# Kernel optimization log

Hardware: AMD Instinct MI355X
Metric: run time of the kernel (lower is better)

The kernel has to match this reference:

```python
import jax, jax.numpy as jnp
import numpy as np
from jax import lax

EPS = 1e-8

def setup_inputs() -> dict:
    key = jax.random.key(0)
    ks = jax.random.split(key, 9)
    B, Cin, H, W = 16, 128, 64, 64
    C = 256
    return {
        "x":  jax.random.normal(ks[0], (B, Cin, H, W), jnp.float32),
        "w1": jax.random.normal(ks[1], (C, Cin, 3, 3), jnp.float32) * 0.02,
        "b1": jax.random.normal(ks[2], (C,), jnp.float32) * 0.02,
        "w2": jax.random.normal(ks[3], (C, C), jnp.float32) * 0.02,
        "b2": jax.random.normal(ks[4], (C,), jnp.float32) * 0.02,
        "w3": jax.random.normal(ks[5], (C, C), jnp.float32) * 0.02,
        "b3": jax.random.normal(ks[6], (C,), jnp.float32) * 0.02,
        "w4": jax.random.normal(ks[7], (C, C), jnp.float32) * 0.02,
        "b4": jax.random.normal(ks[8], (C,), jnp.float32) * 0.02,
    }

def reference(x, w1, b1, w2, b2, w3, b3, w4, b4):
    B = x.shape[0]
    # conv1: 3x3, pad 1 -> [B, 256, H, W]
    conv1 = lax.conv_general_dilated(
        x, w1, window_strides=(1, 1), padding="SAME",
        dimension_numbers=("NCHW", "OIHW", "NCHW")) + b1[None, :, None, None]
    H, W = conv1.shape[2], conv1.shape[3]
    C = conv1.shape[1]
    # gap1 -> [B, 256]; note: forward never applies relu/sigmoid (faithful)
    gap1 = conv1.mean(axis=(2, 3))
    c2 = gap1 @ w2.T + b2            # 1x1 conv on 1x1 spatial == dense
    c3 = c2 @ w3.T + b3              # [B, 256]
    # add1 = conv1 + conv1 * c3 (broadcast scale over spatial)
    add1 = conv1 * (1.0 + c3[:, :, None, None])
    gap2 = add1.mean(axis=(2, 3))    # [B, 256]
    # cosine similarity along channel dim between gap2 and add1 -> [B, H, W]
    num = jnp.einsum("bc,bchw->bhw", gap2, add1)
    n_g = jnp.maximum(jnp.linalg.norm(gap2, axis=1), EPS)[:, None, None]
    n_a = jnp.maximum(jnp.sqrt(jnp.sum(add1 * add1, axis=1)), EPS)
    cos = num / (n_g * n_a)
    r1 = cos.reshape(B, H * W)       # [B, HW]
    m1 = r1.T @ r1                   # [HW, HW] cross-batch position similarity
    # conv4: 1x1 conv -> [B, 256, H, W]
    conv4 = jnp.einsum("oc,bchw->bohw", w4, add1) + b4[None, :, None, None]
    # torch: permute to NHWC then view as [B, 256, HW] (mixes dims; faithful)
    r2 = jnp.transpose(conv4, (0, 2, 3, 1)).reshape(B, C, H * W)
    m2 = r2 @ m1                     # [B, 256, HW]
    return m2.reshape(B, C, H, W)
```

## Files before the change

kernel.cpp:

```cpp
#include <hip/hip_runtime.h>

#define EPSF 1e-8f

typedef __attribute__((ext_vector_type(8))) short bf16x8;
typedef __attribute__((ext_vector_type(16))) float f32x16;

#define MFMA32(a, b, c) __builtin_amdgcn_mfma_f32_32x32x16_bf16(a, b, c, 0, 0, 0)

__device__ __forceinline__ uint32_t splitpack(float v) {
    uint32_t u = __float_as_uint(v);
    uint32_t hb = (u + 0x7fffu + ((u >> 16) & 1u)) & 0xffff0000u;
    float rem = v - __uint_as_float(hb);
    uint32_t r = __float_as_uint(rem);
    uint32_t lb = (r + 0x7fffu + ((r >> 16) & 1u)) >> 16;
    return (hb >> 16) | (lb << 16);
}
__device__ __forceinline__ float unpackf(uint32_t p) {
    return __uint_as_float(p << 16) + __uint_as_float(p & 0xffff0000u);
}

__device__ __forceinline__ void unpack_frag(uint4 a, uint4 b, bf16x8& hi, bf16x8& lo) {
    union { uint32_t w[4]; bf16x8 v; } H, L;
    H.w[0] = (a.x & 0xffffu) | (a.y << 16);
    H.w[1] = (a.z & 0xffffu) | (a.w << 16);
    H.w[2] = (b.x & 0xffffu) | (b.y << 16);
    H.w[3] = (b.z & 0xffffu) | (b.w << 16);
    L.w[0] = (a.x >> 16) | (a.y & 0xffff0000u);
    L.w[1] = (a.z >> 16) | (a.w & 0xffff0000u);
    L.w[2] = (b.x >> 16) | (b.y & 0xffff0000u);
    L.w[3] = (b.z >> 16) | (b.w & 0xffff0000u);
    hi = H.v; lo = L.v;
}

__device__ __forceinline__ void gload_lds16(const void* src, void* dst) {
#if __has_builtin(__builtin_amdgcn_global_load_lds)
    __builtin_amdgcn_global_load_lds(
        (const __attribute__((address_space(1))) uint32_t*)src,
        (__attribute__((address_space(3))) uint32_t*)dst, 16, 0, 0);
#else
    *(uint4*)dst = *(const uint4*)src;
#endif
}

__global__ __launch_bounds__(256) void k_xpack(const float* __restrict__ x,
                                               unsigned short* __restrict__ xph,
                                               unsigned short* __restrict__ xpl) {
    const int bx = blockIdx.x;
    const int hb = bx & 15, cg = (bx >> 4) & 15, b = bx >> 8;
    const int tid = threadIdx.x;
    const int w = tid & 63, hs = tid >> 6;
    const int h = hb * 4 + hs;
    uint32_t hiw[4], low[4];
#pragma unroll
    for (int q = 0; q < 4; ++q) {
        uint32_t u0 = splitpack(x[(((b * 128 + cg * 8 + q * 2) * 64) + h) * 64 + w]);
        uint32_t u1 = splitpack(x[(((b * 128 + cg * 8 + q * 2 + 1) * 64) + h) * 64 + w]);
        hiw[q] = (u0 & 0xffffu) | (u1 << 16);
        low[q] = (u0 >> 16) | (u1 & 0xffff0000u);
    }
    const long o = ((((long)(b * 16 + cg) * 64 + h) * 64) + w) * 8;
    *(uint4*)(xph + o) = *(uint4*)hiw;
    *(uint4*)(xpl + o) = *(uint4*)low;
}

__global__ __launch_bounds__(256) void k_wpack(const float* __restrict__ w1,
                                               short* __restrict__ Bh, short* __restrict__ Bl) {
    int d = blockIdx.x * 256 + threadIdx.x;
    int j = d & 7, lane = (d >> 3) & 63, ot = (d >> 9) & 7, cp = (d >> 12) & 7, tap = d >> 15;
    int oc = ot * 32 + (lane & 31);
    int cin = cp * 16 + (lane >> 5) * 8 + j;
    uint32_t u = splitpack(w1[oc * 1152 + cin * 9 + tap]);
    Bh[d] = (short)(u & 0xffffu);
    Bl[d] = (short)(u >> 16);
}

__global__ __launch_bounds__(256) void k_w4pack(const float* __restrict__ w4,
                                                const float* __restrict__ scale,
                                                short* __restrict__ W4h, short* __restrict__ W4l) {
    int d = blockIdx.x * 256 + threadIdx.x;
    int j = d & 7, lane = (d >> 3) & 63, ot = (d >> 9) & 7;
    int ks = (d >> 12) & 1, cp = (d >> 13) & 7, b = d >> 16;
    int oc = ot * 32 + (lane & 31);
    int c = cp * 32 + ks * 16 + (lane >> 5) * 8 + j;
    uint32_t u = splitpack(w4[oc * 256 + c] * scale[b * 256 + c]);
    W4h[d] = (short)(u & 0xffffu);
    W4l[d] = (short)(u >> 16);
}

__global__ __launch_bounds__(512, 2) void k_conv1(
        const unsigned short* __restrict__ xph, const unsigned short* __restrict__ xpl,
        const short* __restrict__ Bh, const short* __restrict__ Bl,
        const float* __restrict__ b1,
        uint32_t* __restrict__ c1p, float* __restrict__ gpart) {
    __shared__ uint4 lds[2 * 2 * 12 * 66];
    const int bx = blockIdx.x;
    const int oh = bx & 1, hp = (bx >> 1) & 15, b = bx >> 5;
    const int h0 = hp * 4;
    const int tid = threadIdx.x;
    const int lane = tid & 63, wv = tid >> 6;
    const int mq = wv >> 1, nh = wv & 1;
    const int l31 = lane & 31, hbit = lane >> 5;

    f32x16 acc[2][2];
#pragma unroll
    for (int i = 0; i < 2; ++i)
#pragma unroll
        for (int j = 0; j < 2; ++j)
#pragma unroll
            for (int r = 0; r < 16; ++r) acc[i][j][r] = 0.f;

    auto stage = [&](int buf, int cp) {
#pragma unroll
        for (int i = 0; i < 3; ++i) {
            const int id = wv * 3 + i;
            const int plane = (id >= 12) ? 1 : 0;
            const int u = id - plane * 12;
            const int r6 = u >> 1, kg = u & 1;
            const int grow = h0 - 1 + r6;
            uint4* dst = &lds[((buf * 2 + plane) * 12 + u) * 66 + 1 + lane];
            if ((unsigned)grow < 64u) {
                const unsigned short* pls = plane ? xpl : xph;
                const unsigned short* src =
                    pls + ((((long)(b * 16 + cp * 2 + kg) * 64 + grow) * 64) + lane) * 8;
                gload_lds16(src, dst);
            } else {
                *dst = (uint4){0u, 0u, 0u, 0u};
            }
        }
    };

    stage(0, 0);
    if (tid < 96) {
        const int row = tid >> 1, side = tid & 1;
        lds[row * 66 + (side ? 65 : 0)] = (uint4){0u, 0u, 0u, 0u};
    }
    __syncthreads();

    int buf = 0;
    for (int cp = 0; cp < 8; ++cp) {
        if (cp < 7) stage(buf ^ 1, cp + 1);
        bf16x8 Ah[2][2], Al[2][2], Bhv[2][2], Blv[2][2];
#define LOADA(tap, par) do {                                                     \
            const int kh_ = (tap) / 3, kw_ = (tap) % 3;                          \
            _Pragma("unroll")                                                    \
            for (int mt = 0; mt < 2; ++mt) {                                     \
                const int rb = ((buf * 2 + 0) * 12 + (mq + kh_) * 2 + hbit) * 66 \
                               + kw_ + mt * 32 + l31;                            \
                const int rb1 = rb + 12 * 66;                                    \
                Ah[par][mt] = *(const bf16x8*)&lds[rb];                          \
                Al[par][mt] = *(const bf16x8*)&lds[rb1];                         \
            } } while (0)
#define LOADB(tap, par) do {                                                     \
            _Pragma("unroll")                                                    \
            for (int nt = 0; nt < 2; ++nt) {                                     \
                const int fi = (((tap) * 8 + cp) * 8 + oh * 4 + nh * 2 + nt) * 512 + lane * 8; \
                Bhv[par][nt] = *(const bf16x8*)(Bh + fi);                        \
                Blv[par][nt] = *(const bf16x8*)(Bl + fi);                        \
            } } while (0)
        LOADA(0, 0); LOADB(0, 0);
#pragma unroll
        for (int tap = 0; tap < 9; ++tap) {
            const int cur = tap & 1, nxt = cur ^ 1;
            if (tap < 8) { LOADA(tap + 1, nxt); LOADB(tap + 1, nxt); }
#pragma unroll
            for (int nt = 0; nt < 2; ++nt)
#pragma unroll
                for (int mt = 0; mt < 2; ++mt) {
                    acc[mt][nt] = MFMA32(Ah[cur][mt], Bhv[cur][nt], acc[mt][nt]);
                    acc[mt][nt] = MFMA32(Ah[cur][mt], Blv[cur][nt], acc[mt][nt]);
                    acc[mt][nt] = MFMA32(Al[cur][mt], Bhv[cur][nt], acc[mt][nt]);
                }
        }
#undef LOADA
#undef LOADB
        __syncthreads();
        buf ^= 1;
    }

    const int hrow = h0 + mq;
#pragma unroll
    for (int nt = 0; nt < 2; ++nt) {
        const int oc = oh * 128 + nh * 64 + nt * 32 + l31;
        float g = 0.f;
#pragma unroll
        for (int mt = 0; mt < 2; ++mt)
#pragma unroll
            for (int r = 0; r < 16; ++r) g += acc[mt][nt][r];
        g += __shfl_xor(g, 32);
        if (hbit == 0) gpart[((b * 16 + hp) * 4 + mq) * 256 + oc] = g;
        const float bias = b1[oc];
#pragma unroll
        for (int mt = 0; mt < 2; ++mt) {
#pragma unroll
            for (int r = 0; r < 16; ++r) {
                const int row = (r & 3) + 8 * (r >> 2) + 4 * hbit;
                const int p = hrow * 64 + mt * 32 + row;
                c1p[((long)(b * 4096 + p)) * 256 + oc] = splitpack(acc[mt][nt][r] + bias);
            }
        }
    }
}

__global__ __launch_bounds__(256) void k_mlp(const float* __restrict__ gpart,
                                             const float* __restrict__ b1,
                                             const float* __restrict__ w2, const float* __restrict__ b2,
                                             const float* __restrict__ w3, const float* __restrict__ b3,
                                             float* __restrict__ scale, float* __restrict__ ga,
                                             float* __restrict__ n_g) {
    int b = blockIdx.x, tid = threadIdx.x;
    __shared__ float gs[256], c2s[256], red[4];
    float g = 0.f;
#pragma unroll 8
    for (int i = 0; i < 64; ++i) g += gpart[(b * 64 + i) * 256 + tid];
    gs[tid] = g * (1.f / 4096.f) + b1[tid];
    __syncthreads();
    {
        const float4* wr = (const float4*)(w2 + tid * 256);
        float a = b2[tid];
#pragma unroll 8
        for (int c4 = 0; c4 < 64; c4++) {
            float4 wv = wr[c4];
            a += wv.x * gs[c4*4] + wv.y * gs[c4*4+1] + wv.z * gs[c4*4+2] + wv.w * gs[c4*4+3];
        }
        c2s[tid] = a;
    }
    __syncthreads();
    float a3 = b3[tid];
    {
        const float4* wr = (const float4*)(w3 + tid * 256);
#pragma unroll 8
        for (int c4 = 0; c4 < 64; c4++) {
            float4 wv = wr[c4];
            a3 += wv.x * c2s[c4*4] + wv.y * c2s[c4*4+1] + wv.z * c2s[c4*4+2] + wv.w * c2s[c4*4+3];
        }
    }
    float s1 = 1.f + a3;
    float g2 = gs[tid] * s1;
    scale[b * 256 + tid] = s1;
    ga[b * 256 + tid] = g2 * s1;
    float r = g2 * g2;
    for (int off = 32; off; off >>= 1) r += __shfl_down(r, off);
    if ((tid & 63) == 0) red[tid >> 6] = r;
    __syncthreads();
    if (tid == 0) n_g[b] = fmaxf(sqrtf(red[0] + red[1] + red[2] + red[3]), EPSF);
}

__global__ __launch_bounds__(512, 2) void k_conv4(
        const uint32_t* __restrict__ c1p,
        const short* __restrict__ W4h, const short* __restrict__ W4l,
        const float* __restrict__ b4, const float* __restrict__ scale,
        const float* __restrict__ ga, const float* __restrict__ n_g,
        float* __restrict__ outb, float* __restrict__ r1) {
    __shared__ uint4 lds4[2 * 128 * 8];
    __shared__ float scs[256], gas[256];
    __shared__ float cred[128 * 8];
    const int bx = blockIdx.x;
    const int pt = bx & 31, b = bx >> 5;
    const int p0 = pt * 128;
    const int tid = threadIdx.x;
    const int lane = tid & 63, wv = tid >> 6;
    const int mhalf = wv >> 2, nq = wv & 3;
    const int l31 = lane & 31, hbit = lane >> 5;
    const int pc = tid & 127, cq = tid >> 7;
    const float ng = n_g[b];

    if (tid < 256) { scs[tid] = scale[b * 256 + tid]; gas[tid] = ga[b * 256 + tid]; }

    f32x16 acc[2][2];
#pragma unroll
    for (int i = 0; i < 2; ++i)
#pragma unroll
        for (int j = 0; j < 2; ++j)
#pragma unroll
            for (int r = 0; r < 16; ++r) acc[i][j][r] = 0.f;

    const int qsrc = (lane & 7) ^ (lane >> 3);
    auto stage = [&](int buf, int cp) {
#pragma unroll
        for (int i = 0; i < 2; ++i) {
            const int id = wv * 2 + i;
            const int pbase = id * 8;
            const uint32_t* src = c1p + ((long)(b * 4096 + p0 + pbase + (lane >> 3))) * 256
                                  + cp * 32 + qsrc * 4;
            uint4* dst = &lds4[buf * 1024 + pbase * 8 + lane];
            gload_lds16(src, dst);
        }
    };

    stage(0, 0);
    __syncthreads();

    float cnum = 0.f, cden = 0.f;
    int buf = 0;
    for (int cp = 0; cp < 8; ++cp) {
        if (cp < 7) stage(buf ^ 1, cp + 1);
        {
            uint4 a = lds4[buf * 1024 + pc * 8 + ((cq * 2) ^ (pc & 7))];
            uint4 bq = lds4[buf * 1024 + pc * 8 + ((cq * 2 + 1) ^ (pc & 7))];
            uint32_t pk[8] = {a.x, a.y, a.z, a.w, bq.x, bq.y, bq.z, bq.w};
#pragma unroll
            for (int j = 0; j < 8; ++j) {
                const float v = unpackf(pk[j]);
                const int c = cp * 32 + cq * 8 + j;
                cnum += gas[c] * v;
                const float t = scs[c] * v;
                cden += t * t;
            }
        }
        bf16x8 Wh[2][2], Wl[2][2];
#define LOADW(cp_, ks_, par) do {                                                \
            _Pragma("unroll")                                                    \
            for (int nt = 0; nt < 2; ++nt) {                                     \
                const int fi = ((((b * 8 + (cp_)) * 2 + (ks_)) * 8) + nq * 2 + nt) * 512 + lane * 8; \
                Wh[par][nt] = *(const bf16x8*)(W4h + fi);                        \
                Wl[par][nt] = *(const bf16x8*)(W4l + fi);                        \
            } } while (0)
        LOADW(cp, 0, 0);
#pragma unroll
        for (int ks = 0; ks < 2; ++ks) {
            if (ks == 0) LOADW(cp, 1, 1);
            bf16x8 ah[2], al[2];
#pragma unroll
            for (int mt = 0; mt < 2; ++mt) {
                const int pidx = mhalf * 64 + mt * 32 + l31;
                const int g = ks * 2 + hbit;
                uint4 ua = lds4[buf * 1024 + pidx * 8 + ((g * 2) ^ (pidx & 7))];
                uint4 ub = lds4[buf * 1024 + pidx * 8 + ((g * 2 + 1) ^ (pidx & 7))];
                unpack_frag(ua, ub, ah[mt], al[mt]);
            }
#pragma unroll
            for (int nt = 0; nt < 2; ++nt)
#pragma unroll
                for (int mt = 0; mt < 2; ++mt) {
                    acc[mt][nt] = MFMA32(ah[mt], Wh[ks][nt], acc[mt][nt]);
                    acc[mt][nt] = MFMA32(ah[mt], Wl[ks][nt], acc[mt][nt]);
                    acc[mt][nt] = MFMA32(al[mt], Wh[ks][nt], acc[mt][nt]);
                }
        }
#undef LOADW
        __syncthreads();
        buf ^= 1;
    }

    cred[pc * 8 + cq] = cnum;
    cred[pc * 8 + 4 + cq] = cden;
    __syncthreads();
    if (tid < 128) {
        const float n = cred[tid * 8] + cred[tid * 8 + 1] + cred[tid * 8 + 2] + cred[tid * 8 + 3];
        const float d = cred[tid * 8 + 4] + cred[tid * 8 + 5] + cred[tid * 8 + 6] + cred[tid * 8 + 7];
        r1[b * 4096 + p0 + tid] = n / (fmaxf(sqrtf(d), EPSF) * ng);
    }

#pragma unroll
    for (int nt = 0; nt < 2; ++nt) {
        const int o = nq * 64 + nt * 32 + l31;
        const float bias = b4[o];
#pragma unroll
        for (int mt = 0; mt < 2; ++mt) {
#pragma unroll
            for (int r = 0; r < 16; ++r) {
                const int row = (r & 3) + 8 * (r >> 2) + 4 * hbit;
                const int p = p0 + mhalf * 64 + mt * 32 + row;
                outb[((long)(b * 4096 + p)) * 256 + o] = acc[mt][nt][r] + bias;
            }
        }
    }
}

__global__ __launch_bounds__(256) void k_t(const float* __restrict__ outb,
                                           const float* __restrict__ r1,
                                           float* __restrict__ tmat) {
    __shared__ float r2c[16][256];
    __shared__ float r1c[16][260];
    int bx = blockIdx.x; int b = bx >> 4, it = bx & 15;
    int tid = threadIdx.x;
    int il = tid >> 4, bp = tid & 15;
    float acc = 0.f;
    for (int jc = 0; jc < 4096; jc += 256) {
        __syncthreads();
#pragma unroll
        for (int k = 0; k < 4; k++) {
            int f4i = tid + k * 256;
            int row = f4i >> 6, col = f4i & 63;
            *(float4*)&r2c[row][col * 4] =
                *(const float4*)(outb + ((long)b << 20) + ((long)(it * 16 + row) << 12) + jc + col * 4);
            *(float4*)&r1c[row][col * 4] =
                *(const float4*)(r1 + ((long)row << 12) + jc + col * 4);
        }
        __syncthreads();
#pragma unroll 8
        for (int j = 0; j < 256; j += 4) {
            float4 a4  = *(const float4*)&r2c[il][j];
            float4 b4v = *(const float4*)&r1c[bp][j];
            acc += a4.x * b4v.x + a4.y * b4v.y + a4.z * b4v.z + a4.w * b4v.w;
        }
    }
    tmat[((b * 256) + it * 16 + il) * 16 + bp] = acc;
}

__global__ __launch_bounds__(256) void k_m2(const float* __restrict__ tmat,
                                            const float* __restrict__ r1,
                                            float* __restrict__ outb) {
    __shared__ float r1s[16][512];
    __shared__ float ts[256];
    int bx = blockIdx.x;
    int b = bx >> 7, it = (bx >> 3) & 15, pc = bx & 7;
    int tid = threadIdx.x;
    ts[tid] = tmat[(b * 256 + it * 16) * 16 + tid];
#pragma unroll
    for (int k = 0; k < 8; k++) {
        int f4i = tid + k * 256;
        int row = f4i >> 7, col = f4i & 127;
        *(float4*)&r1s[row][col * 4] = *(const float4*)(r1 + ((long)row << 12) + pc * 512 + col * 4);
    }
    __syncthreads();
    for (int il = 0; il < 16; il++) {
        float tv[16];
#pragma unroll
        for (int bp = 0; bp < 16; bp++) tv[bp] = ts[il * 16 + bp];
#pragma unroll
        for (int k = 0; k < 2; k++) {
            int p = k * 256 + tid;
            float s = 0.f;
#pragma unroll
            for (int bp = 0; bp < 16; bp++) s += tv[bp] * r1s[bp][p];
            outb[((long)b << 20) + ((long)(it * 16 + il) << 12) + pc * 512 + p] = s;
        }
    }
}

extern "C" void kernel_launch(void* const* d_in, const int* in_sizes, int n_in,
                              void* d_out, int out_size, void* d_ws, size_t ws_size,
                              hipStream_t stream) {
    const float* x  = (const float*)d_in[0];
    const float* w1 = (const float*)d_in[1];
    const float* b1 = (const float*)d_in[2];
    const float* w2 = (const float*)d_in[3];
    const float* b2 = (const float*)d_in[4];
    const float* w3 = (const float*)d_in[5];
    const float* b3 = (const float*)d_in[6];
    const float* w4 = (const float*)d_in[7];
    const float* b4 = (const float*)d_in[8];
    float* out = (float*)d_out;

    unsigned short* xph = (unsigned short*)d_out;
    unsigned short* xpl = xph + 8388608L;

    char* p = (char*)d_ws;
    uint32_t* c1p = (uint32_t*)p;  p += 16777216L * 4;
    short* Bh  = (short*)p;  p += 294912L * 2;
    short* Bl  = (short*)p;  p += 294912L * 2;
    short* W4h = (short*)p;  p += 1048576L * 2;
    short* W4l = (short*)p;  p += 1048576L * 2;
    float* gpart = (float*)p; p += 262144L * 4;
    float* scale = (float*)p; p += 4096L * 4;
    float* ga    = (float*)p; p += 4096L * 4;
    float* n_g   = (float*)p; p += 16L * 4;
    float* r1    = (float*)p; p += 65536L * 4;
    float* tmat  = (float*)p; p += 65536L * 4;

    k_xpack <<<4096, 256, 0, stream>>>(x, xph, xpl);
    k_wpack <<<1152, 256, 0, stream>>>(w1, Bh, Bl);
    k_conv1 <<<512,  512, 0, stream>>>(xph, xpl, Bh, Bl, b1, c1p, gpart);
    k_mlp   <<<16,   256, 0, stream>>>(gpart, b1, w2, b2, w3, b3, scale, ga, n_g);
    k_w4pack<<<4096, 256, 0, stream>>>(w4, scale, W4h, W4l);
    k_conv4 <<<512,  512, 0, stream>>>(c1p, W4h, W4l, b4, scale, ga, n_g, out, r1);
    k_t     <<<256,  256, 0, stream>>>(out, r1, tmat);
    k_m2    <<<2048, 256, 0, stream>>>(tmat, r1, out);
}
```

Baseline: 251.2 us.

## Eliminate conv4 GEMM by reassociating w4 into r1-side projection; retile conv1

```diff
diff --git a/kernel.cpp b/kernel.cpp
--- a/kernel.cpp
+++ b/kernel.cpp
@@ -17,19 +17,6 @@
 }
 __device__ __forceinline__ float unpackf(uint32_t p) {
     return __uint_as_float(p << 16) + __uint_as_float(p & 0xffff0000u);
-}
-
-__device__ __forceinline__ void unpack_frag(uint4 a, uint4 b, bf16x8& hi, bf16x8& lo) {
-    union { uint32_t w[4]; bf16x8 v; } H, L;
-    H.w[0] = (a.x & 0xffffu) | (a.y << 16);
-    H.w[1] = (a.z & 0xffffu) | (a.w << 16);
-    H.w[2] = (b.x & 0xffffu) | (b.y << 16);
-    H.w[3] = (b.z & 0xffffu) | (b.w << 16);
-    L.w[0] = (a.x >> 16) | (a.y & 0xffff0000u);
-    L.w[1] = (a.z >> 16) | (a.w & 0xffff0000u);
-    L.w[2] = (b.x >> 16) | (b.y & 0xffff0000u);
-    L.w[3] = (b.z >> 16) | (b.w & 0xffff0000u);
-    hi = H.v; lo = L.v;
 }
 
 __device__ __forceinline__ void gload_lds16(const void* src, void* dst) {
@@ -66,48 +53,33 @@
 __global__ __launch_bounds__(256) void k_wpack(const float* __restrict__ w1,
                                                short* __restrict__ Bh, short* __restrict__ Bl) {
     int d = blockIdx.x * 256 + threadIdx.x;
-    int j = d & 7, lane = (d >> 3) & 63, ot = (d >> 9) & 7, cp = (d >> 12) & 7, tap = d >> 15;
-    int oc = ot * 32 + (lane & 31);
+    int j = d & 7, lane = (d >> 3) & 63, nt = (d >> 9) & 7, cp = (d >> 12) & 7, tap = d >> 15;
+    int oc = nt * 32 + (lane & 31);
     int cin = cp * 16 + (lane >> 5) * 8 + j;
     uint32_t u = splitpack(w1[oc * 1152 + cin * 9 + tap]);
     Bh[d] = (short)(u & 0xffffu);
     Bl[d] = (short)(u >> 16);
 }
 
-__global__ __launch_bounds__(256) void k_w4pack(const float* __restrict__ w4,
-                                                const float* __restrict__ scale,
-                                                short* __restrict__ W4h, short* __restrict__ W4l) {
-    int d = blockIdx.x * 256 + threadIdx.x;
-    int j = d & 7, lane = (d >> 3) & 63, ot = (d >> 9) & 7;
-    int ks = (d >> 12) & 1, cp = (d >> 13) & 7, b = d >> 16;
-    int oc = ot * 32 + (lane & 31);
-    int c = cp * 32 + ks * 16 + (lane >> 5) * 8 + j;
-    uint32_t u = splitpack(w4[oc * 256 + c] * scale[b * 256 + c]);
-    W4h[d] = (short)(u & 0xffffu);
-    W4l[d] = (short)(u >> 16);
-}
-
-__global__ __launch_bounds__(512, 2) void k_conv1(
+__global__ __launch_bounds__(512, 4) void k_conv1(
         const unsigned short* __restrict__ xph, const unsigned short* __restrict__ xpl,
         const short* __restrict__ Bh, const short* __restrict__ Bl,
         const float* __restrict__ b1,
         uint32_t* __restrict__ c1p, float* __restrict__ gpart) {
     __shared__ uint4 lds[2 * 2 * 12 * 66];
     const int bx = blockIdx.x;
-    const int oh = bx & 1, hp = (bx >> 1) & 15, b = bx >> 5;
+    const int ot = bx & 3, hp = (bx >> 2) & 15, b = bx >> 6;
     const int h0 = hp * 4;
     const int tid = threadIdx.x;
     const int lane = tid & 63, wv = tid >> 6;
     const int mq = wv >> 1, nh = wv & 1;
     const int l31 = lane & 31, hbit = lane >> 5;
 
-    f32x16 acc[2][2];
+    f32x16 acc[2];
 #pragma unroll
     for (int i = 0; i < 2; ++i)
 #pragma unroll
-        for (int j = 0; j < 2; ++j)
-#pragma unroll
-            for (int r = 0; r < 16; ++r) acc[i][j][r] = 0.f;
+        for (int r = 0; r < 16; ++r) acc[i][r] = 0.f;
 
     auto stage = [&](int buf, int cp) {
 #pragma unroll
@@ -139,7 +111,7 @@
     int buf = 0;
     for (int cp = 0; cp < 8; ++cp) {
         if (cp < 7) stage(buf ^ 1, cp + 1);
-        bf16x8 Ah[2][2], Al[2][2], Bhv[2][2], Blv[2][2];
+        bf16x8 Ah[2][2], Al[2][2], Bhv[2], Blv[2];
 #define LOADA(tap, par) do {                                                     \
             const int kh_ = (tap) / 3, kw_ = (tap) % 3;                          \
             _Pragma("unroll")                                                    \
@@ -151,25 +123,23 @@
                 Al[par][mt] = *(const bf16x8*)&lds[rb1];                         \
             } } while (0)
 #define LOADB(tap, par) do {                                                     \
-            _Pragma("unroll")                                                    \
-            for (int nt = 0; nt < 2; ++nt) {                                     \
-                const int fi = (((tap) * 8 + cp) * 8 + oh * 4 + nh * 2 + nt) * 512 + lane * 8; \
-                Bhv[par][nt] = *(const bf16x8*)(Bh + fi);                        \
-                Blv[par][nt] = *(const bf16x8*)(Bl + fi);                        \
-            } } while (0)
+            const int fi = (((tap) * 8 + cp) * 8 + ot * 2 + nh) * 512 + lane * 8; \
+            Bhv[par] = *(const bf16x8*)(Bh + fi);                                \
+            Blv[par] = *(const bf16x8*)(Bl + fi);                                \
+        } while (0)
         LOADA(0, 0); LOADB(0, 0);
 #pragma unroll
         for (int tap = 0; tap < 9; ++tap) {
             const int cur = tap & 1, nxt = cur ^ 1;
             if (tap < 8) { LOADA(tap + 1, nxt); LOADB(tap + 1, nxt); }
-#pragma unroll
-            for (int nt = 0; nt < 2; ++nt)
-#pragma unroll
-                for (int mt = 0; mt < 2; ++mt) {
-                    acc[mt][nt] = MFMA32(Ah[cur][mt], Bhv[cur][nt], acc[mt][nt]);
-                    acc[mt][nt] = MFMA32(Ah[cur][mt], Blv[cur][nt], acc[mt][nt]);
-                    acc[mt][nt] = MFMA32(Al[cur][mt], Bhv[cur][nt], acc[mt][nt]);
-                }
+            __builtin_amdgcn_s_setprio(1);
+#pragma unroll
+            for (int mt = 0; mt < 2; ++mt) {
+                acc[mt] = MFMA32(Ah[cur][mt], Bhv[cur], acc[mt]);
+                acc[mt] = MFMA32(Ah[cur][mt], Blv[cur], acc[mt]);
+                acc[mt] = MFMA32(Al[cur][mt], Bhv[cur], acc[mt]);
+            }
+            __builtin_amdgcn_s_setprio(0);
         }
 #undef LOADA
 #undef LOADB
@@ -178,25 +148,24 @@
     }
 
     const int hrow = h0 + mq;
-#pragma unroll
-    for (int nt = 0; nt < 2; ++nt) {
-        const int oc = oh * 128 + nh * 64 + nt * 32 + l31;
+    const int oc = ot * 64 + nh * 32 + l31;
+    {
         float g = 0.f;
 #pragma unroll
         for (int mt = 0; mt < 2; ++mt)
 #pragma unroll
-            for (int r = 0; r < 16; ++r) g += acc[mt][nt][r];
+            for (int r = 0; r < 16; ++r) g += acc[mt][r];
         g += __shfl_xor(g, 32);
         if (hbit == 0) gpart[((b * 16 + hp) * 4 + mq) * 256 + oc] = g;
-        const float bias = b1[oc];
-#pragma unroll
-        for (int mt = 0; mt < 2; ++mt) {
-#pragma unroll
-            for (int r = 0; r < 16; ++r) {
-                const int row = (r & 3) + 8 * (r >> 2) + 4 * hbit;
-                const int p = hrow * 64 + mt * 32 + row;
-                c1p[((long)(b * 4096 + p)) * 256 + oc] = splitpack(acc[mt][nt][r] + bias);
-            }
+    }
+    const float bias = b1[oc];
+#pragma unroll
+    for (int mt = 0; mt < 2; ++mt) {
+#pragma unroll
+        for (int r = 0; r < 16; ++r) {
+            const int row = (r & 3) + 8 * (r >> 2) + 4 * hbit;
+            const int p = hrow * 64 + mt * 32 + row;
+            c1p[((long)(b * 4096 + p)) * 256 + oc] = splitpack(acc[mt][r] + bias);
         }
     }
 }
@@ -245,157 +214,110 @@
     if (tid == 0) n_g[b] = fmaxf(sqrtf(red[0] + red[1] + red[2] + red[3]), EPSF);
 }
 
-__global__ __launch_bounds__(512, 2) void k_conv4(
+__global__ __launch_bounds__(256) void k_cos(
         const uint32_t* __restrict__ c1p,
-        const short* __restrict__ W4h, const short* __restrict__ W4l,
-        const float* __restrict__ b4, const float* __restrict__ scale,
-        const float* __restrict__ ga, const float* __restrict__ n_g,
-        float* __restrict__ outb, float* __restrict__ r1) {
-    __shared__ uint4 lds4[2 * 128 * 8];
-    __shared__ float scs[256], gas[256];
-    __shared__ float cred[128 * 8];
+        const float* __restrict__ scale, const float* __restrict__ ga,
+        const float* __restrict__ n_g, float* __restrict__ r1) {
     const int bx = blockIdx.x;
-    const int pt = bx & 31, b = bx >> 5;
-    const int p0 = pt * 128;
+    const int pt = bx & 63, b = bx >> 6;
     const int tid = threadIdx.x;
     const int lane = tid & 63, wv = tid >> 6;
-    const int mhalf = wv >> 2, nq = wv & 3;
-    const int l31 = lane & 31, hbit = lane >> 5;
-    const int pc = tid & 127, cq = tid >> 7;
+    const int half = lane >> 5, l31 = lane & 31;
+    float ga8[8], sc8[8];
+#pragma unroll
+    for (int q = 0; q < 8; ++q) {
+        ga8[q] = ga[b * 256 + l31 * 8 + q];
+        sc8[q] = scale[b * 256 + l31 * 8 + q];
+    }
     const float ng = n_g[b];
-
-    if (tid < 256) { scs[tid] = scale[b * 256 + tid]; gas[tid] = ga[b * 256 + tid]; }
-
-    f32x16 acc[2][2];
-#pragma unroll
-    for (int i = 0; i < 2; ++i)
-#pragma unroll
-        for (int j = 0; j < 2; ++j)
-#pragma unroll
-            for (int r = 0; r < 16; ++r) acc[i][j][r] = 0.f;
-
-    const int qsrc = (lane & 7) ^ (lane >> 3);
-    auto stage = [&](int buf, int cp) {
-#pragma unroll
-        for (int i = 0; i < 2; ++i) {
-            const int id = wv * 2 + i;
-            const int pbase = id * 8;
-            const uint32_t* src = c1p + ((long)(b * 4096 + p0 + pbase + (lane >> 3))) * 256
-                                  + cp * 32 + qsrc * 4;
-            uint4* dst = &lds4[buf * 1024 + pbase * 8 + lane];
-            gload_lds16(src, dst);
-        }
-    };
-
-    stage(0, 0);
-    __syncthreads();
-
-    float cnum = 0.f, cden = 0.f;
-    int buf = 0;
-    for (int cp = 0; cp < 8; ++cp) {
-        if (cp < 7) stage(buf ^ 1, cp + 1);
-        {
-            uint4 a = lds4[buf * 1024 + pc * 8 + ((cq * 2) ^ (pc & 7))];
-            uint4 bq = lds4[buf * 1024 + pc * 8 + ((cq * 2 + 1) ^ (pc & 7))];
-            uint32_t pk[8] = {a.x, a.y, a.z, a.w, bq.x, bq.y, bq.z, bq.w};
-#pragma unroll
-            for (int j = 0; j < 8; ++j) {
-                const float v = unpackf(pk[j]);
-                const int c = cp * 32 + cq * 8 + j;
-                cnum += gas[c] * v;
-                const float t = scs[c] * v;
-                cden += t * t;
-            }
-        }
-        bf16x8 Wh[2][2], Wl[2][2];
-#define LOADW(cp_, ks_, par) do {                                                \
-            _Pragma("unroll")                                                    \
-            for (int nt = 0; nt < 2; ++nt) {                                     \
-                const int fi = ((((b * 8 + (cp_)) * 2 + (ks_)) * 8) + nq * 2 + nt) * 512 + lane * 8; \
-                Wh[par][nt] = *(const bf16x8*)(W4h + fi);                        \
-                Wl[par][nt] = *(const bf16x8*)(W4l + fi);                        \
-            } } while (0)
-        LOADW(cp, 0, 0);
-#pragma unroll
-        for (int ks = 0; ks < 2; ++ks) {
-            if (ks == 0) LOADW(cp, 1, 1);
-            bf16x8 ah[2], al[2];
-#pragma unroll
-            for (int mt = 0; mt < 2; ++mt) {
-                const int pidx = mhalf * 64 + mt * 32 + l31;
-                const int g = ks * 2 + hbit;
-                uint4 ua = lds4[buf * 1024 + pidx * 8 + ((g * 2) ^ (pidx & 7))];
-                uint4 ub = lds4[buf * 1024 + pidx * 8 + ((g * 2 + 1) ^ (pidx & 7))];
-                unpack_frag(ua, ub, ah[mt], al[mt]);
-            }
-#pragma unroll
-            for (int nt = 0; nt < 2; ++nt)
-#pragma unroll
-                for (int mt = 0; mt < 2; ++mt) {
-                    acc[mt][nt] = MFMA32(ah[mt], Wh[ks][nt], acc[mt][nt]);
-                    acc[mt][nt] = MFMA32(ah[mt], Wl[ks][nt], acc[mt][nt]);
-                    acc[mt][nt] = MFMA32(al[mt], Wh[ks][nt], acc[mt][nt]);
-                }
-        }
-#undef LOADW
+#pragma unroll
+    for (int pp = 0; pp < 8; ++pp) {
+        const int p = pt * 64 + wv * 16 + pp * 2 + half;
+        const uint32_t* base = c1p + ((long)(b * 4096 + p)) * 256 + l31 * 8;
+        uint4 a = *(const uint4*)base;
+        uint4 bq = *(const uint4*)(base + 4);
+        uint32_t pk[8] = {a.x, a.y, a.z, a.w, bq.x, bq.y, bq.z, bq.w};
+        float num = 0.f, den = 0.f;
+#pragma unroll
+        for (int q = 0; q < 8; ++q) {
+            const float v = unpackf(pk[q]);
+            num += ga8[q] * v;
+            const float t = sc8[q] * v;
+            den += t * t;
+        }
+#pragma unroll
+        for (int off = 1; off <= 16; off <<= 1) {
+            num += __shfl_xor(num, off);
+            den += __shfl_xor(den, off);
+        }
+        if (l31 == 0) {
+            float na = fmaxf(sqrtf(den), EPSF);
+            r1[b * 4096 + p] = num / (ng * na);
+        }
+    }
+}
+
+__global__ __launch_bounds__(256) void k_u(const float* __restrict__ r1,
+                                           const float* __restrict__ w4,
+                                           const float* __restrict__ b4,
+                                           float* __restrict__ Uf, float* __restrict__ Dpart) {
+    const int g = blockIdx.x;
+    const int tid = threadIdx.x;
+    __shared__ float rs[256], red[4];
+    rs[tid] = r1[(g >> 4) * 4096 + (g & 15) * 256 + tid];
+    __syncthreads();
+    float a = 0.f;
+#pragma unroll 8
+    for (int o = 0; o < 256; ++o) a += rs[o] * w4[o * 256 + tid];
+    Uf[(g >> 4) * 4096 + (g & 15) * 256 + tid] = a;
+    float d = b4[tid] * rs[tid];
+    for (int off = 32; off; off >>= 1) d += __shfl_down(d, off);
+    if ((tid & 63) == 0) red[tid >> 6] = d;
+    __syncthreads();
+    if (tid == 0) Dpart[g] = red[0] + red[1] + red[2] + red[3];
+}
+
+__global__ __launch_bounds__(256) void k_t2(const uint32_t* __restrict__ c1p,
+                                            const float* __restrict__ Uf,
+                                            const float* __restrict__ scale,
+                                            const float* __restrict__ Dpart,
+                                            float* __restrict__ tmat) {
+    __shared__ float Ac[16][256];
+    __shared__ float Bc[16][260];
+    __shared__ float scs[256];
+    const int bx = blockIdx.x;
+    const int b = bx >> 4, it = bx & 15;
+    const int tid = threadIdx.x;
+    const int il = tid >> 4, bp = tid & 15;
+    scs[tid] = scale[b * 256 + tid];
+    float acc = 0.f;
+    for (int jc = 0; jc < 16; ++jc) {
         __syncthreads();
-        buf ^= 1;
-    }
-
-    cred[pc * 8 + cq] = cnum;
-    cred[pc * 8 + 4 + cq] = cden;
-    __syncthreads();
-    if (tid < 128) {
-        const float n = cred[tid * 8] + cred[tid * 8 + 1] + cred[tid * 8 + 2] + cred[tid * 8 + 3];
-        const float d = cred[tid * 8 + 4] + cred[tid * 8 + 5] + cred[tid * 8 + 6] + cred[tid * 8 + 7];
-        r1[b * 4096 + p0 + tid] = n / (fmaxf(sqrtf(d), EPSF) * ng);
-    }
-
-#pragma unroll
-    for (int nt = 0; nt < 2; ++nt) {
-        const int o = nq * 64 + nt * 32 + l31;
-        const float bias = b4[o];
-#pragma unroll
-        for (int mt = 0; mt < 2; ++mt) {
-#pragma unroll
-            for (int r = 0; r < 16; ++r) {
-                const int row = (r & 3) + 8 * (r >> 2) + 4 * hbit;
-                const int p = p0 + mhalf * 64 + mt * 32 + row;
-                outb[((long)(b * 4096 + p)) * 256 + o] = acc[mt][nt][r] + bias;
-            }
-        }
-    }
-}
-
-__global__ __launch_bounds__(256) void k_t(const float* __restrict__ outb,
-                                           const float* __restrict__ r1,
-                                           float* __restrict__ tmat) {
-    __shared__ float r2c[16][256];
-    __shared__ float r1c[16][260];
-    int bx = blockIdx.x; int b = bx >> 4, it = bx & 15;
-    int tid = threadIdx.x;
-    int il = tid >> 4, bp = tid & 15;
-    float acc = 0.f;
-    for (int jc = 0; jc < 4096; jc += 256) {
+#pragma unroll
+        for (int q = 0; q < 4; ++q) {
+            const int f4i = tid + q * 256;
+            const int row = f4i >> 6, col4 = f4i & 63;
+            uint4 u = *(const uint4*)(c1p +
+                ((long)(b * 4096 + it * 256 + row * 16 + jc)) * 256 + col4 * 4);
+            Ac[row][col4 * 4 + 0] = unpackf(u.x) * scs[col4 * 4 + 0];
+            Ac[row][col4 * 4 + 1] = unpackf(u.y) * scs[col4 * 4 + 1];
+            Ac[row][col4 * 4 + 2] = unpackf(u.z) * scs[col4 * 4 + 2];
+            Ac[row][col4 * 4 + 3] = unpackf(u.w) * scs[col4 * 4 + 3];
+            *(float4*)&Bc[row][col4 * 4] =
+                *(const float4*)(Uf + (long)row * 4096 + jc * 256 + col4 * 4);
+        }
         __syncthreads();
-#pragma unroll
-        for (int k = 0; k < 4; k++) {
-            int f4i = tid + k * 256;
-            int row = f4i >> 6, col = f4i & 63;
-            *(float4*)&r2c[row][col * 4] =
-                *(const float4*)(outb + ((long)b << 20) + ((long)(it * 16 + row) << 12) + jc + col * 4);
-            *(float4*)&r1c[row][col * 4] =
-                *(const float4*)(r1 + ((long)row << 12) + jc + col * 4);
-        }
-        __syncthreads();
 #pragma unroll 8
         for (int j = 0; j < 256; j += 4) {
-            float4 a4  = *(const float4*)&r2c[il][j];
-            float4 b4v = *(const float4*)&r1c[bp][j];
+            float4 a4  = *(const float4*)&Ac[il][j];
+            float4 b4v = *(const float4*)&Bc[bp][j];
             acc += a4.x * b4v.x + a4.y * b4v.y + a4.z * b4v.z + a4.w * b4v.w;
         }
     }
-    tmat[((b * 256) + it * 16 + il) * 16 + bp] = acc;
+    float D = 0.f;
+#pragma unroll
+    for (int pr = 0; pr < 16; ++pr) D += Dpart[bp * 16 + pr];
+    tmat[((b * 256) + it * 16 + il) * 16 + bp] = acc + D;
 }
 
 __global__ __launch_bounds__(256) void k_m2(const float* __restrict__ tmat,
@@ -450,21 +372,21 @@
     uint32_t* c1p = (uint32_t*)p;  p += 16777216L * 4;
     short* Bh  = (short*)p;  p += 294912L * 2;
     short* Bl  = (short*)p;  p += 294912L * 2;
-    short* W4h = (short*)p;  p += 1048576L * 2;
-    short* W4l = (short*)p;  p += 1048576L * 2;
     float* gpart = (float*)p; p += 262144L * 4;
     float* scale = (float*)p; p += 4096L * 4;
     float* ga    = (float*)p; p += 4096L * 4;
     float* n_g   = (float*)p; p += 16L * 4;
     float* r1    = (float*)p; p += 65536L * 4;
     float* tmat  = (float*)p; p += 65536L * 4;
+    float* Uf    = (float*)p; p += 65536L * 4;
+    float* Dpart = (float*)p; p += 256L * 4;
 
     k_xpack <<<4096, 256, 0, stream>>>(x, xph, xpl);
     k_wpack <<<1152, 256, 0, stream>>>(w1, Bh, Bl);
-    k_conv1 <<<512,  512, 0, stream>>>(xph, xpl, Bh, Bl, b1, c1p, gpart);
+    k_conv1 <<<1024, 512, 0, stream>>>(xph, xpl, Bh, Bl, b1, c1p, gpart);
     k_mlp   <<<16,   256, 0, stream>>>(gpart, b1, w2, b2, w3, b3, scale, ga, n_g);
-    k_w4pack<<<4096, 256, 0, stream>>>(w4, scale, W4h, W4l);
-    k_conv4 <<<512,  512, 0, stream>>>(c1p, W4h, W4l, b4, scale, ga, n_g, out, r1);
-    k_t     <<<256,  256, 0, stream>>>(out, r1, tmat);
+    k_cos   <<<1024, 256, 0, stream>>>(c1p, scale, ga, n_g, r1);
+    k_u     <<<256,  256, 0, stream>>>(r1, w4, b4, Uf, Dpart);
+    k_t2    <<<256,  256, 0, stream>>>(c1p, Uf, scale, Dpart, tmat);
     k_m2    <<<2048, 256, 0, stream>>>(tmat, r1, out);
 }
```

After: 243.7 us. 3.0% less time.
